# Kernel optimization log

Hardware: AMD Instinct MI355X
Metric: run time of the kernel (lower is better)

## Reference

```python
import jax, jax.numpy as jnp
import numpy as np

N_ENT = 100000
N_USR = 1024
E = 400000
D = 128
H = 4
R = 32


def setup_inputs() -> dict:
    key = jax.random.key(0)
    ks = jax.random.split(key, 9)
    a = float(np.sqrt(6.0 / (D + D)))  # xavier_uniform bound for [D, D]
    return {
        "entity_emb": jax.random.normal(ks[0], (N_ENT, D), dtype=jnp.float32),
        "user_emb": jax.random.normal(ks[1], (N_USR, D), dtype=jnp.float32),
        "interact_mat": jnp.zeros((1,), dtype=jnp.float32),  # unused by forward
        "weight": jax.random.normal(ks[2], (R, D), dtype=jnp.float32) * 0.1,
        "qTrans": jax.random.uniform(ks[3], (D, D), minval=-a, maxval=a, dtype=jnp.float32),
        "kTrans": jax.random.uniform(ks[4], (D, D), minval=-a, maxval=a, dtype=jnp.float32),
        "vTrans": jax.random.uniform(ks[5], (D, D), minval=-a, maxval=a, dtype=jnp.float32),
        "edge_index": jax.random.randint(ks[6], (2, E), 0, N_ENT, dtype=jnp.int64)
            if jax.config.jax_enable_x64 else jax.random.randint(ks[6], (2, E), 0, N_ENT, dtype=jnp.int32),
        "edge_type": jax.random.randint(ks[7], (E,), 1, R + 1, dtype=jnp.int32),  # types in [1, R]
        "layer": 0,
    }


def _kglayer(rows, col_embeds, embeds, n_seg, qT, kT, vT):
    # rows: [E] target-node index, col_embeds: [E, D] edge messages
    dh = D // H
    row_embeds = embeds[rows]                              # gather [E, D]
    q = (row_embeds @ qT).reshape(-1, H, dh)
    k = (col_embeds @ kT).reshape(-1, H, dh)
    v = (col_embeds @ vT).reshape(-1, H, dh)
    att = jnp.clip(jnp.einsum("ehd,ehd->eh", q, k), -10.0, 10.0)
    exp_att = jnp.exp(att)                                 # [E, H]
    att_norm = jax.ops.segment_sum(exp_att, rows, num_segments=n_seg)[rows]
    att = exp_att / (att_norm + 1e-8)
    res = (att[..., None] * v).reshape(-1, D)              # [E, D]
    return jax.ops.segment_sum(res, rows, num_segments=n_seg)


def _sim_hrt(head_emb, tail_emb, rel_emb):
    # per-edge scalar attention logit [E, 1]
    tr = jnp.linalg.norm(tail_emb * rel_emb, axis=1, keepdims=True)
    hr = jnp.linalg.norm(head_emb * rel_emb, axis=1, keepdims=True)
    return (hr * tr) ** 2


def reference(entity_emb, user_emb, interact_mat, weight, qTrans, kTrans, vTrans,
              edge_index, edge_type, layer):
    n_entities = entity_emb.shape[0]
    head, tail = edge_index[0], edge_index[1]
    rel = weight[edge_type - 1]                            # [E, D]
    neigh = entity_emb[tail] * rel                         # [E, D]
    kg_emb = _kglayer(head, neigh, entity_emb, n_entities, qTrans, kTrans, vTrans)
    w = _sim_hrt(kg_emb[head], kg_emb[tail], rel)          # [E, 1]
    w = jnp.broadcast_to(w, neigh.shape)                   # expand to [E, D]
    # scatter_softmax over edges sharing the same head (numerically stable)
    m = jax.ops.segment_max(w, head, num_segments=n_entities)[head]
    e = jnp.exp(w - m)
    s = jax.ops.segment_sum(e, head, num_segments=n_entities)[head]
    soft = e / s
    msg = soft * entity_emb[tail]
    return jax.ops.segment_sum(msg, head, num_segments=n_entities)
```

## Files before the change

### kernel.cpp

```cpp
#include <hip/hip_runtime.h>
#include <cstdint>

#define D 128
#define H 4
#define N_ENT 100000
#define N_EDGE 400000
#define R 32

#define SCAN_NB ((N_ENT + 511) / 512)

__global__ void k_hist(const int* __restrict__ head, int* __restrict__ deg) {
  const int e = blockIdx.x * 256 + threadIdx.x;
  if (e < N_EDGE) atomicAdd(&deg[head[e]], 1);
}

__global__ __launch_bounds__(256) void k_scan1(const int* __restrict__ deg,
                                               int* __restrict__ bsum) {
  const int t = threadIdx.x;
  const int i = blockIdx.x * 512 + t * 2;
  int v0 = (i < N_ENT) ? deg[i] : 0;
  int v1 = (i + 1 < N_ENT) ? deg[i + 1] : 0;
  int s = v0 + v1;
#pragma unroll
  for (int k = 1; k < 64; k <<= 1) s += __shfl_xor(s, k);
  __shared__ int ws[4];
  if ((t & 63) == 0) ws[t >> 6] = s;
  __syncthreads();
  if (t == 0) bsum[blockIdx.x] = ws[0] + ws[1] + ws[2] + ws[3];
}

__global__ __launch_bounds__(256) void k_scan2(const int* __restrict__ bsum,
                                               int* __restrict__ bbase,
                                               int* __restrict__ off) {
  __shared__ int sh[256];
  const int t = threadIdx.x;
  const int v = (t < SCAN_NB) ? bsum[t] : 0;
  sh[t] = v;
  __syncthreads();
  for (int d = 1; d < 256; d <<= 1) {
    const int u = (t >= d) ? sh[t - d] : 0;
    __syncthreads();
    sh[t] += u;
    __syncthreads();
  }
  if (t < SCAN_NB) bbase[t] = sh[t] - v;
  if (t == SCAN_NB - 1) off[N_ENT] = sh[t];
}

__global__ __launch_bounds__(256) void k_scan3(const int* __restrict__ deg,
                                               const int* __restrict__ bbase,
                                               int* __restrict__ off,
                                               int* __restrict__ cur) {
  __shared__ int sh[256];
  const int t = threadIdx.x;
  const int i = blockIdx.x * 512 + t * 2;
  const int v0 = (i < N_ENT) ? deg[i] : 0;
  const int v1 = (i + 1 < N_ENT) ? deg[i + 1] : 0;
  const int s = v0 + v1;
  sh[t] = s;
  __syncthreads();
  for (int d = 1; d < 256; d <<= 1) {
    const int u = (t >= d) ? sh[t - d] : 0;
    __syncthreads();
    sh[t] += u;
    __syncthreads();
  }
  const int ex = sh[t] - s + bbase[blockIdx.x];
  if (i < N_ENT) {
    off[i] = ex;
    cur[i] = ex;
  }
  if (i + 1 < N_ENT) {
    off[i + 1] = ex + v0;
    cur[i + 1] = ex + v0;
  }
}

__global__ void k_scatter(const int* __restrict__ head,
                          const int* __restrict__ tail,
                          const int* __restrict__ etype, int* __restrict__ cur,
                          int2* __restrict__ teP) {
  const int e = blockIdx.x * 256 + threadIdx.x;
  if (e >= N_EDGE) return;
  const int hd = head[e];
  const int pos = atomicAdd(&cur[hd], 1);
  teP[pos] = make_int2(tail[e], etype[e] - 1);
}

__global__ __launch_bounds__(256) void k_tr(const float* __restrict__ in,
                                            float* __restrict__ out) {
  __shared__ float tile[32][33];
  const int bx = blockIdx.x & 3, by = blockIdx.x >> 2;
  const int c = threadIdx.x & 31;
  const int r0 = (threadIdx.x >> 5) * 4;
#pragma unroll
  for (int i = 0; i < 4; ++i)
    tile[r0 + i][c] = in[(by * 32 + r0 + i) * 128 + bx * 32 + c];
  __syncthreads();
#pragma unroll
  for (int i = 0; i < 4; ++i)
    out[(bx * 32 + r0 + i) * 128 + by * 32 + c] = tile[c][r0 + i];
}

__global__ __launch_bounds__(512) void k_qproj(const float* __restrict__ ent,
                                               const float* __restrict__ qT,
                                               float* __restrict__ Q) {
  __shared__ float sT[D * D];
  __shared__ float rows[D * 128];
  const int t = threadIdx.x;
  const int n0 = blockIdx.x * 128;
#pragma unroll
  for (int s = 0; s < 8; ++s) {
    const int idx = (s * 512 + t) * 4;
    *(float4*)&sT[idx] = *(const float4*)&qT[idx];
  }
  {
    const int g = t & 3;
    const int n = t >> 2;
    const int node = n0 + n;
    if (node < N_ENT) {
      const float* src = ent + (size_t)node * D;
#pragma unroll
      for (int s = 0; s < 8; ++s) {
        const int i = s * 16 + g * 4;
        float4 v = *(const float4*)&src[i];
        rows[(i + 0) * 128 + n] = v.x;
        rows[(i + 1) * 128 + n] = v.y;
        rows[(i + 2) * 128 + n] = v.z;
        rows[(i + 3) * 128 + n] = v.w;
      }
    } else {
#pragma unroll
      for (int s = 0; s < 8; ++s) {
        const int i = s * 16 + g * 4;
        rows[(i + 0) * 128 + n] = 0.f;
        rows[(i + 1) * 128 + n] = 0.f;
        rows[(i + 2) * 128 + n] = 0.f;
        rows[(i + 3) * 128 + n] = 0.f;
      }
    }
  }
  __syncthreads();
  const int jj = t & 15;
  const int ee = t >> 4;
  float acc[4][8];
#pragma unroll
  for (int a = 0; a < 4; ++a)
#pragma unroll
    for (int b = 0; b < 8; ++b) acc[a][b] = 0.f;
#pragma unroll 4
  for (int i = 0; i < D; ++i) {
    float4 b0 = *(float4*)&sT[i * D + jj * 8];
    float4 b1 = *(float4*)&sT[i * D + jj * 8 + 4];
    float4 a0 = *(float4*)&rows[i * 128 + ee * 4];
    float bv[8] = {b0.x, b0.y, b0.z, b0.w, b1.x, b1.y, b1.z, b1.w};
    float av[4] = {a0.x, a0.y, a0.z, a0.w};
#pragma unroll
    for (int a = 0; a < 4; ++a)
#pragma unroll
      for (int b = 0; b < 8; ++b) acc[a][b] = fmaf(av[a], bv[b], acc[a][b]);
  }
#pragma unroll
  for (int a = 0; a < 4; ++a) {
    const int node = n0 + ee * 4 + a;
    if (node < N_ENT) {
      float4 o0 = {acc[a][0], acc[a][1], acc[a][2], acc[a][3]};
      float4 o1 = {acc[a][4], acc[a][5], acc[a][6], acc[a][7]};
      *(float4*)&Q[(size_t)node * D + jj * 8] = o0;
      *(float4*)&Q[(size_t)node * D + jj * 8 + 4] = o1;
    }
  }
}

__global__ __launch_bounds__(256, 8) void k_fused(
    const float* __restrict__ ent, const float* __restrict__ wrel,
    const float* __restrict__ kTt, const float* __restrict__ vT, float* qkg,
    const int* __restrict__ off, const int2* __restrict__ teP) {
  __shared__ float sQ[8 * 128];
  __shared__ float sPA[8 * 512];
  const int t = threadIdx.x;
  const int base = blockIdx.x * 8;

  const int wid = t >> 6;
  const int half = (t >> 5) & 1;
  const int l32 = t & 31;
  const int kk = wid * 2 + half;
  const int n = base + kk;

  {
    const int k = t >> 5;
    const int c4 = (t & 31) * 4;
    *(float4*)&sQ[k * 128 + c4] =
        *(const float4*)&qkg[(size_t)(base + k) * D + c4];
  }

  const int eb = off[n];
  const int deg = off[n + 1] - eb;
  float4 xv = {0, 0, 0, 0}, rv = {0, 0, 0, 0};
  if (deg > 0) {
    const int2 pf = teP[eb];
    xv = *(const float4*)&ent[(size_t)pf.x * D + l32 * 4];
    rv = *(const float4*)&wrel[(size_t)pf.y * D + l32 * 4];
  }
  __syncthreads();

  {
    const int i = t & 127;
    const int sub = t >> 7;
    float pp[2][8];
#pragma unroll
    for (int hh = 0; hh < 2; ++hh)
#pragma unroll
      for (int k = 0; k < 8; ++k) pp[hh][k] = 0.f;
#pragma unroll
    for (int hh = 0; hh < 2; ++hh) {
      const int h = sub * 2 + hh;
#pragma unroll 2
      for (int c4 = 0; c4 < 8; ++c4) {
        const float kv0 = kTt[(h * 32 + c4 * 4 + 0) * 128 + i];
        const float kv1 = kTt[(h * 32 + c4 * 4 + 1) * 128 + i];
        const float kv2 = kTt[(h * 32 + c4 * 4 + 2) * 128 + i];
        const float kv3 = kTt[(h * 32 + c4 * 4 + 3) * 128 + i];
#pragma unroll
        for (int k = 0; k < 8; ++k) {
          const float4 q = *(const float4*)&sQ[k * 128 + h * 32 + c4 * 4];
          pp[hh][k] = fmaf(kv0, q.x, pp[hh][k]);
          pp[hh][k] = fmaf(kv1, q.y, pp[hh][k]);
          pp[hh][k] = fmaf(kv2, q.z, pp[hh][k]);
          pp[hh][k] = fmaf(kv3, q.w, pp[hh][k]);
        }
      }
    }
#pragma unroll
    for (int hh = 0; hh < 2; ++hh)
#pragma unroll
      for (int k = 0; k < 8; ++k)
        sPA[k * 512 + (sub * 2 + hh) * 128 + i] = pp[hh][k];
  }
  __syncthreads();

  {
    const int lp = l32 & 3;
    const float4 P0 = *(const float4*)&sPA[kk * 512 + 0 * 128 + l32 * 4];
    const float4 P1 = *(const float4*)&sPA[kk * 512 + 1 * 128 + l32 * 4];
    const float4 P2 = *(const float4*)&sPA[kk * 512 + 2 * 128 + l32 * 4];
    const float4 P3 = *(const float4*)&sPA[kk * 512 + 3 * 128 + l32 * 4];
    float4 b0 = {0, 0, 0, 0}, b1 = {0, 0, 0, 0};
    float4 b2 = {0, 0, 0, 0}, b3 = {0, 0, 0, 0};
    float s0 = 0.f, s1 = 0.f, s2 = 0.f, s3 = 0.f;
    for (int idx = 0; idx < deg; ++idx) {
      const float4 cx = xv, cr = rv;
      if (idx + 1 < deg) {
        const int2 pf = teP[eb + idx + 1];
        xv = *(const float4*)&ent[(size_t)pf.x * D + l32 * 4];
        rv = *(const float4*)&wrel[(size_t)pf.y * D + l32 * 4];
      }
      const float4 nh = {cx.x * cr.x, cx.y * cr.y, cx.z * cr.z, cx.w * cr.w};
      float d0 = nh.x * P0.x + nh.y * P0.y + nh.z * P0.z + nh.w * P0.w;
      float d1 = nh.x * P1.x + nh.y * P1.y + nh.z * P1.z + nh.w * P1.w;
      float d2 = nh.x * P2.x + nh.y * P2.y + nh.z * P2.z + nh.w * P2.w;
      float d3 = nh.x * P3.x + nh.y * P3.y + nh.z * P3.z + nh.w * P3.w;
      float x01 = (l32 & 1) ? d1 : d0;
      float y01 = (l32 & 1) ? d0 : d1;
      x01 += __shfl_xor(y01, 1);
      float x23 = (l32 & 1) ? d3 : d2;
      float y23 = (l32 & 1) ? d2 : d3;
      x23 += __shfl_xor(y23, 1);
      float xa = (l32 & 2) ? x23 : x01;
      float xb = (l32 & 2) ? x01 : x23;
      xa += __shfl_xor(xb, 2);
      xa += __shfl_xor(xa, 4);
      xa += __shfl_xor(xa, 8);
      xa += __shfl_xor(xa, 16);
      const float eL = __expf(fminf(fmaxf(xa, -10.f), 10.f));
      const float e0 = eL;
      const float e1 = __shfl_xor(eL, 1);
      const float e2 = __shfl_xor(eL, 2);
      const float e3 = __shfl_xor(eL, 3);
      b0.x = fmaf(e0, nh.x, b0.x); b0.y = fmaf(e0, nh.y, b0.y);
      b0.z = fmaf(e0, nh.z, b0.z); b0.w = fmaf(e0, nh.w, b0.w);
      b1.x = fmaf(e1, nh.x, b1.x); b1.y = fmaf(e1, nh.y, b1.y);
      b1.z = fmaf(e1, nh.z, b1.z); b1.w = fmaf(e1, nh.w, b1.w);
      b2.x = fmaf(e2, nh.x, b2.x); b2.y = fmaf(e2, nh.y, b2.y);
      b2.z = fmaf(e2, nh.z, b2.z); b2.w = fmaf(e2, nh.w, b2.w);
      b3.x = fmaf(e3, nh.x, b3.x); b3.y = fmaf(e3, nh.y, b3.y);
      b3.z = fmaf(e3, nh.z, b3.z); b3.w = fmaf(e3, nh.w, b3.w);
      s0 += e0; s1 += e1; s2 += e2; s3 += e3;
    }
    const float i0 = 1.f / (s0 + 1e-8f);
    const float i1 = 1.f / (s1 + 1e-8f);
    const float i2 = 1.f / (s2 + 1e-8f);
    const float i3 = 1.f / (s3 + 1e-8f);
    float4 o0 = {b0.x * i0, b0.y * i0, b0.z * i0, b0.w * i0};
    float4 o1 = {b1.x * i1, b1.y * i1, b1.z * i1, b1.w * i1};
    float4 o2 = {b2.x * i2, b2.y * i2, b2.z * i2, b2.w * i2};
    float4 o3 = {b3.x * i3, b3.y * i3, b3.z * i3, b3.w * i3};
    const int sb = kk * 512 + l32 * 4;
    *(float4*)&sPA[sb + ((lp ^ 0) << 7)] = o0;
    *(float4*)&sPA[sb + ((lp ^ 1) << 7)] = o1;
    *(float4*)&sPA[sb + ((lp ^ 2) << 7)] = o2;
    *(float4*)&sPA[sb + ((lp ^ 3) << 7)] = o3;
  }
  __syncthreads();

  {
    const int c = t & 127;
    const int g4 = (t >> 7) * 4;
    const int h = c >> 5;
    float acc0 = 0.f, acc1 = 0.f, acc2 = 0.f, acc3 = 0.f;
    const float* agg0 = &sPA[(g4 + 0) * 512 + h * 128];
    const float* agg1 = &sPA[(g4 + 1) * 512 + h * 128];
    const float* agg2 = &sPA[(g4 + 2) * 512 + h * 128];
    const float* agg3 = &sPA[(g4 + 3) * 512 + h * 128];
#pragma unroll 4
    for (int d4 = 0; d4 < 32; ++d4) {
      const float4 a0 = *(const float4*)&agg0[d4 * 4];
      const float4 a1 = *(const float4*)&agg1[d4 * 4];
      const float4 a2 = *(const float4*)&agg2[d4 * 4];
      const float4 a3 = *(const float4*)&agg3[d4 * 4];
      const float v0 = vT[(d4 * 4 + 0) * 128 + c];
      const float v1 = vT[(d4 * 4 + 1) * 128 + c];
      const float v2 = vT[(d4 * 4 + 2) * 128 + c];
      const float v3 = vT[(d4 * 4 + 3) * 128 + c];
      acc0 = fmaf(a0.x, v0, acc0); acc0 = fmaf(a0.y, v1, acc0);
      acc0 = fmaf(a0.z, v2, acc0); acc0 = fmaf(a0.w, v3, acc0);
      acc1 = fmaf(a1.x, v0, acc1); acc1 = fmaf(a1.y, v1, acc1);
      acc1 = fmaf(a1.z, v2, acc1); acc1 = fmaf(a1.w, v3, acc1);
      acc2 = fmaf(a2.x, v0, acc2); acc2 = fmaf(a2.y, v1, acc2);
      acc2 = fmaf(a2.z, v2, acc2); acc2 = fmaf(a2.w, v3, acc2);
      acc3 = fmaf(a3.x, v0, acc3); acc3 = fmaf(a3.y, v1, acc3);
      acc3 = fmaf(a3.z, v2, acc3); acc3 = fmaf(a3.w, v3, acc3);
    }
    qkg[(size_t)(base + g4 + 0) * D + c] = acc0;
    qkg[(size_t)(base + g4 + 1) * D + c] = acc1;
    qkg[(size_t)(base + g4 + 2) * D + c] = acc2;
    qkg[(size_t)(base + g4 + 3) * D + c] = acc3;
  }
}

__global__ __launch_bounds__(256) void k_S(const float* __restrict__ kg,
                                           const float* __restrict__ wrel,
                                           float* __restrict__ S) {
  __shared__ float sB[D * 32];
  __shared__ float sA[D * 64];
  const int t = threadIdx.x;
  const int n0 = blockIdx.x * 64;
  {
    const int r = t & 31;
    const int qg = t >> 5;
#pragma unroll
    for (int s = 0; s < 4; ++s) {
      const int d = qg * 16 + s * 4;
      float4 b = *(const float4*)&wrel[(size_t)r * D + d];
      sB[(d + 0) * 32 + r] = b.x * b.x;
      sB[(d + 1) * 32 + r] = b.y * b.y;
      sB[(d + 2) * 32 + r] = b.z * b.z;
      sB[(d + 3) * 32 + r] = b.w * b.w;
    }
  }
  {
    const int nn = t & 63;
    const int dg = t >> 6;
    const int node = n0 + nn;
#pragma unroll
    for (int s = 0; s < 8; ++s) {
      const int d = dg * 32 + s * 4;
      float4 a = {0, 0, 0, 0};
      if (node < N_ENT) a = *(const float4*)&kg[(size_t)node * D + d];
      sA[(d + 0) * 64 + nn] = a.x * a.x;
      sA[(d + 1) * 64 + nn] = a.y * a.y;
      sA[(d + 2) * 64 + nn] = a.z * a.z;
      sA[(d + 3) * 64 + nn] = a.w * a.w;
    }
  }
  __syncthreads();
  const int nn2 = t >> 2;
  const int rg = t & 3;
  float acc[8];
#pragma unroll
  for (int c = 0; c < 8; ++c) acc[c] = 0.f;
#pragma unroll 4
  for (int d = 0; d < D; ++d) {
    const float a = sA[d * 64 + nn2];
    float4 b0 = *(float4*)&sB[d * 32 + rg * 8];
    float4 b1 = *(float4*)&sB[d * 32 + rg * 8 + 4];
    acc[0] = fmaf(a, b0.x, acc[0]);
    acc[1] = fmaf(a, b0.y, acc[1]);
    acc[2] = fmaf(a, b0.z, acc[2]);
    acc[3] = fmaf(a, b0.w, acc[3]);
    acc[4] = fmaf(a, b1.x, acc[4]);
    acc[5] = fmaf(a, b1.y, acc[5]);
    acc[6] = fmaf(a, b1.z, acc[6]);
    acc[7] = fmaf(a, b1.w, acc[7]);
  }
  const int node = n0 + nn2;
  if (node < N_ENT) {
    float4 o0 = {acc[0], acc[1], acc[2], acc[3]};
    float4 o1 = {acc[4], acc[5], acc[6], acc[7]};
    *(float4*)&S[(size_t)node * 32 + rg * 8] = o0;
    *(float4*)&S[(size_t)node * 32 + rg * 8 + 4] = o1;
  }
}

__global__ __launch_bounds__(256) void k_out2(
    const float* __restrict__ ent, const float* __restrict__ S,
    const int* __restrict__ off, const int2* __restrict__ teP,
    float* __restrict__ out) {
  const int t = threadIdx.x;
  const int wid = t >> 6;
  const int lane = t & 63;
  const int n = blockIdx.x * 4 + wid;
  if (n >= N_ENT) return;
  const int eb = off[n];
  const int deg = off[n + 1] - eb;
  float accx = 0.f, accy = 0.f;
  float m = 0.f, ssum = 0.f;
  for (int b = 0; b < deg; b += 64) {
    const int idx = b + lane;
    const bool val = idx < deg;
    const int e = eb + (val ? idx : 0);
    const int2 tp = teP[e];
    const int tl = tp.x;
    const int ty = tp.y;
    float w = val ? S[(size_t)n * 32 + ty] * S[(size_t)tl * 32 + ty] : -1.f;
    float cm = w;
#pragma unroll
    for (int k = 1; k < 64; k <<= 1) cm = fmaxf(cm, __shfl_xor(cm, k));
    const float mnew = fmaxf(m, cm);
    const float scale = __expf(m - mnew);
    const float el = val ? __expf(w - mnew) : 0.f;
    float cs = el;
#pragma unroll
    for (int k = 1; k < 64; k <<= 1) cs += __shfl_xor(cs, k);
    ssum = ssum * scale + cs;
    accx *= scale;
    accy *= scale;
    const int cnt = (deg - b < 64) ? deg - b : 64;
    {
      const int tl0 = __shfl(tl, 0);
      float2 xr = *(const float2*)&ent[(size_t)tl0 * D + lane * 2];
      for (int j = 0; j < cnt; ++j) {
        const float sj = __shfl(el, j);
        const float2 cx = xr;
        if (j + 1 < cnt) {
          const int tlj = __shfl(tl, j + 1);
          xr = *(const float2*)&ent[(size_t)tlj * D + lane * 2];
        }
        accx = fmaf(sj, cx.x, accx);
        accy = fmaf(sj, cx.y, accy);
      }
    }
    m = mnew;
  }
  const float inv = (deg > 0) ? 1.f / ssum : 0.f;
  float2 o = {accx * inv, accy * inv};
  *(float2*)&out[(size_t)n * D + lane * 2] = o;
}

extern "C" void kernel_launch(void* const* d_in, const int* in_sizes, int n_in,
                              void* d_out, int out_size, void* d_ws,
                              size_t ws_size, hipStream_t stream) {
  const float* ent = (const float*)d_in[0];
  const float* wrel = (const float*)d_in[3];
  const float* qT = (const float*)d_in[4];
  const float* kT = (const float*)d_in[5];
  const float* vT = (const float*)d_in[6];
  const int* eidx = (const int*)d_in[7];
  const int* etype = (const int*)d_in[8];
  const int* head = eidx;
  const int* tail = eidx + N_EDGE;

  float* S = (float*)d_ws;
  int* off = (int*)(S + (size_t)N_ENT * 32);
  int* cur = off + (N_ENT + 2);
  int* deg = cur + N_ENT;
  int* bsum = deg + N_ENT;
  int* bbase = bsum + SCAN_NB;
  int2* teP = (int2*)(bbase + SCAN_NB);
  float* kTt = (float*)(teP + N_EDGE);
  float* qkg = (float*)d_out;

  hipMemsetAsync(deg, 0, N_ENT * sizeof(int), stream);
  k_hist<<<(N_EDGE + 255) / 256, 256, 0, stream>>>(head, deg);
  k_scan1<<<SCAN_NB, 256, 0, stream>>>(deg, bsum);
  k_scan2<<<1, 256, 0, stream>>>(bsum, bbase, off);
  k_scan3<<<SCAN_NB, 256, 0, stream>>>(deg, bbase, off, cur);
  k_scatter<<<(N_EDGE + 255) / 256, 256, 0, stream>>>(head, tail, etype, cur,
                                                      teP);
  k_tr<<<16, 256, 0, stream>>>(kT, kTt);
  k_qproj<<<(N_ENT + 127) / 128, 512, 0, stream>>>(ent, qT, qkg);
  k_fused<<<N_ENT / 8, 256, 0, stream>>>(ent, wrel, kTt, vT, qkg, off, teP);
  k_S<<<(N_ENT + 63) / 64, 256, 0, stream>>>(qkg, wrel, S);
  k_out2<<<(N_ENT + 3) / 4, 256, 0, stream>>>(ent, S, off, teP, qkg);
}
```

Baseline: 512.1 us.

## Fuse Q projection and relation-score kernel into main fused attention kernel

Removes the separate Q-projection kernel and the S (kg²·rel²) kernel and computes both inside k_fused per block of 8 nodes. Q is computed from entity rows in shared memory using qT read from global, and S is computed right after kg from squared values kept in shared memory. A small prep kernel transposes kT and precomputes squared relation weights. This avoids writing Q and kg to global and reading them back, plus two launches. In exchange k_fused does more per-block work with global qT reads, and its occupancy hint drops from 8 to 4 blocks.

Result: slower. 577.7 us (+12.8%).

```diff
diff --git a/kernel.cpp b/kernel.cpp
--- a/kernel.cpp
+++ b/kernel.cpp
@@ -87,95 +87,40 @@
   teP[pos] = make_int2(tail[e], etype[e] - 1);
 }
 
-__global__ __launch_bounds__(256) void k_tr(const float* __restrict__ in,
-                                            float* __restrict__ out) {
-  __shared__ float tile[32][33];
-  const int bx = blockIdx.x & 3, by = blockIdx.x >> 2;
-  const int c = threadIdx.x & 31;
-  const int r0 = (threadIdx.x >> 5) * 4;
-#pragma unroll
-  for (int i = 0; i < 4; ++i)
-    tile[r0 + i][c] = in[(by * 32 + r0 + i) * 128 + bx * 32 + c];
-  __syncthreads();
-#pragma unroll
-  for (int i = 0; i < 4; ++i)
-    out[(bx * 32 + r0 + i) * 128 + by * 32 + c] = tile[c][r0 + i];
-}
-
-__global__ __launch_bounds__(512) void k_qproj(const float* __restrict__ ent,
-                                               const float* __restrict__ qT,
-                                               float* __restrict__ Q) {
-  __shared__ float sT[D * D];
-  __shared__ float rows[D * 128];
-  const int t = threadIdx.x;
-  const int n0 = blockIdx.x * 128;
-#pragma unroll
-  for (int s = 0; s < 8; ++s) {
-    const int idx = (s * 512 + t) * 4;
-    *(float4*)&sT[idx] = *(const float4*)&qT[idx];
-  }
-  {
-    const int g = t & 3;
-    const int n = t >> 2;
-    const int node = n0 + n;
-    if (node < N_ENT) {
-      const float* src = ent + (size_t)node * D;
-#pragma unroll
-      for (int s = 0; s < 8; ++s) {
-        const int i = s * 16 + g * 4;
-        float4 v = *(const float4*)&src[i];
-        rows[(i + 0) * 128 + n] = v.x;
-        rows[(i + 1) * 128 + n] = v.y;
-        rows[(i + 2) * 128 + n] = v.z;
-        rows[(i + 3) * 128 + n] = v.w;
-      }
-    } else {
-#pragma unroll
-      for (int s = 0; s < 8; ++s) {
-        const int i = s * 16 + g * 4;
-        rows[(i + 0) * 128 + n] = 0.f;
-        rows[(i + 1) * 128 + n] = 0.f;
-        rows[(i + 2) * 128 + n] = 0.f;
-        rows[(i + 3) * 128 + n] = 0.f;
-      }
-    }
-  }
-  __syncthreads();
-  const int jj = t & 15;
-  const int ee = t >> 4;
-  float acc[4][8];
-#pragma unroll
-  for (int a = 0; a < 4; ++a)
-#pragma unroll
-    for (int b = 0; b < 8; ++b) acc[a][b] = 0.f;
-#pragma unroll 4
-  for (int i = 0; i < D; ++i) {
-    float4 b0 = *(float4*)&sT[i * D + jj * 8];
-    float4 b1 = *(float4*)&sT[i * D + jj * 8 + 4];
-    float4 a0 = *(float4*)&rows[i * 128 + ee * 4];
-    float bv[8] = {b0.x, b0.y, b0.z, b0.w, b1.x, b1.y, b1.z, b1.w};
-    float av[4] = {a0.x, a0.y, a0.z, a0.w};
-#pragma unroll
-    for (int a = 0; a < 4; ++a)
-#pragma unroll
-      for (int b = 0; b < 8; ++b) acc[a][b] = fmaf(av[a], bv[b], acc[a][b]);
-  }
-#pragma unroll
-  for (int a = 0; a < 4; ++a) {
-    const int node = n0 + ee * 4 + a;
-    if (node < N_ENT) {
-      float4 o0 = {acc[a][0], acc[a][1], acc[a][2], acc[a][3]};
-      float4 o1 = {acc[a][4], acc[a][5], acc[a][6], acc[a][7]};
-      *(float4*)&Q[(size_t)node * D + jj * 8] = o0;
-      *(float4*)&Q[(size_t)node * D + jj * 8 + 4] = o1;
-    }
-  }
-}
-
-__global__ __launch_bounds__(256, 8) void k_fused(
+__global__ __launch_bounds__(256) void k_prep(const float* __restrict__ kT,
+                                              float* __restrict__ kTt,
+                                              const float* __restrict__ wrel,
+                                              float* __restrict__ wrel2) {
+  if (blockIdx.x < 16) {
+    __shared__ float tile[32][33];
+    const int bx = blockIdx.x & 3, by = blockIdx.x >> 2;
+    const int c = threadIdx.x & 31;
+    const int r0 = (threadIdx.x >> 5) * 4;
+#pragma unroll
+    for (int i = 0; i < 4; ++i)
+      tile[r0 + i][c] = kT[(by * 32 + r0 + i) * 128 + bx * 32 + c];
+    __syncthreads();
+#pragma unroll
+    for (int i = 0; i < 4; ++i)
+      kTt[(bx * 32 + r0 + i) * 128 + by * 32 + c] = tile[c][r0 + i];
+  } else {
+    const int t = threadIdx.x;
+#pragma unroll
+    for (int s = 0; s < 4; ++s) {
+      const int idx = (s * 256 + t) * 4;
+      float4 v = *(const float4*)&wrel[idx];
+      v.x *= v.x; v.y *= v.y; v.z *= v.z; v.w *= v.w;
+      *(float4*)&wrel2[idx] = v;
+    }
+  }
+}
+
+__global__ __launch_bounds__(256, 4) void k_fused(
     const float* __restrict__ ent, const float* __restrict__ wrel,
-    const float* __restrict__ kTt, const float* __restrict__ vT, float* qkg,
-    const int* __restrict__ off, const int2* __restrict__ teP) {
+    const float* __restrict__ qT, const float* __restrict__ kTt,
+    const float* __restrict__ vT, const float* __restrict__ wrel2,
+    float* __restrict__ S, const int* __restrict__ off,
+    const int2* __restrict__ teP) {
   __shared__ float sQ[8 * 128];
   __shared__ float sPA[8 * 512];
   const int t = threadIdx.x;
@@ -190,8 +135,8 @@
   {
     const int k = t >> 5;
     const int c4 = (t & 31) * 4;
-    *(float4*)&sQ[k * 128 + c4] =
-        *(const float4*)&qkg[(size_t)(base + k) * D + c4];
+    *(float4*)&sPA[k * 128 + c4] =
+        *(const float4*)&ent[(size_t)(base + k) * D + c4];
   }
 
   const int eb = off[n];
@@ -201,6 +146,40 @@
     const int2 pf = teP[eb];
     xv = *(const float4*)&ent[(size_t)pf.x * D + l32 * 4];
     rv = *(const float4*)&wrel[(size_t)pf.y * D + l32 * 4];
+  }
+  __syncthreads();
+
+  {
+    const int j = t & 127;
+    const int g4 = (t >> 7) * 4;
+    const float* sE0 = &sPA[(g4 + 0) * 128];
+    const float* sE1 = &sPA[(g4 + 1) * 128];
+    const float* sE2 = &sPA[(g4 + 2) * 128];
+    const float* sE3 = &sPA[(g4 + 3) * 128];
+    float q0 = 0.f, q1 = 0.f, q2 = 0.f, q3 = 0.f;
+#pragma unroll 4
+    for (int c4 = 0; c4 < 32; ++c4) {
+      const float4 e0 = *(const float4*)&sE0[c4 * 4];
+      const float4 e1 = *(const float4*)&sE1[c4 * 4];
+      const float4 e2 = *(const float4*)&sE2[c4 * 4];
+      const float4 e3 = *(const float4*)&sE3[c4 * 4];
+      const float t0 = qT[(c4 * 4 + 0) * 128 + j];
+      const float t1 = qT[(c4 * 4 + 1) * 128 + j];
+      const float t2 = qT[(c4 * 4 + 2) * 128 + j];
+      const float t3 = qT[(c4 * 4 + 3) * 128 + j];
+      q0 = fmaf(e0.x, t0, q0); q0 = fmaf(e0.y, t1, q0);
+      q0 = fmaf(e0.z, t2, q0); q0 = fmaf(e0.w, t3, q0);
+      q1 = fmaf(e1.x, t0, q1); q1 = fmaf(e1.y, t1, q1);
+      q1 = fmaf(e1.z, t2, q1); q1 = fmaf(e1.w, t3, q1);
+      q2 = fmaf(e2.x, t0, q2); q2 = fmaf(e2.y, t1, q2);
+      q2 = fmaf(e2.z, t2, q2); q2 = fmaf(e2.w, t3, q2);
+      q3 = fmaf(e3.x, t0, q3); q3 = fmaf(e3.y, t1, q3);
+      q3 = fmaf(e3.z, t2, q3); q3 = fmaf(e3.w, t3, q3);
+    }
+    sQ[(g4 + 0) * 128 + j] = q0;
+    sQ[(g4 + 1) * 128 + j] = q1;
+    sQ[(g4 + 2) * 128 + j] = q2;
+    sQ[(g4 + 3) * 128 + j] = q3;
   }
   __syncthreads();
 
@@ -231,6 +210,7 @@
         }
       }
     }
+    __syncthreads();
 #pragma unroll
     for (int hh = 0; hh < 2; ++hh)
 #pragma unroll
@@ -249,13 +229,12 @@
     float4 b2 = {0, 0, 0, 0}, b3 = {0, 0, 0, 0};
     float s0 = 0.f, s1 = 0.f, s2 = 0.f, s3 = 0.f;
     for (int idx = 0; idx < deg; ++idx) {
-      const float4 cx = xv, cr = rv;
+      const float4 nh = {xv.x * rv.x, xv.y * rv.y, xv.z * rv.z, xv.w * rv.w};
       if (idx + 1 < deg) {
         const int2 pf = teP[eb + idx + 1];
         xv = *(const float4*)&ent[(size_t)pf.x * D + l32 * 4];
         rv = *(const float4*)&wrel[(size_t)pf.y * D + l32 * 4];
       }
-      const float4 nh = {cx.x * cr.x, cx.y * cr.y, cx.z * cr.z, cx.w * cr.w};
       float d0 = nh.x * P0.x + nh.y * P0.y + nh.z * P0.z + nh.w * P0.w;
       float d1 = nh.x * P1.x + nh.y * P1.y + nh.z * P1.z + nh.w * P1.w;
       float d2 = nh.x * P2.x + nh.y * P2.y + nh.z * P2.z + nh.w * P2.w;
@@ -331,74 +310,27 @@
       acc3 = fmaf(a3.x, v0, acc3); acc3 = fmaf(a3.y, v1, acc3);
       acc3 = fmaf(a3.z, v2, acc3); acc3 = fmaf(a3.w, v3, acc3);
     }
-    qkg[(size_t)(base + g4 + 0) * D + c] = acc0;
-    qkg[(size_t)(base + g4 + 1) * D + c] = acc1;
-    qkg[(size_t)(base + g4 + 2) * D + c] = acc2;
-    qkg[(size_t)(base + g4 + 3) * D + c] = acc3;
-  }
-}
-
-__global__ __launch_bounds__(256) void k_S(const float* __restrict__ kg,
-                                           const float* __restrict__ wrel,
-                                           float* __restrict__ S) {
-  __shared__ float sB[D * 32];
-  __shared__ float sA[D * 64];
-  const int t = threadIdx.x;
-  const int n0 = blockIdx.x * 64;
-  {
+    sQ[(g4 + 0) * 128 + c] = acc0 * acc0;
+    sQ[(g4 + 1) * 128 + c] = acc1 * acc1;
+    sQ[(g4 + 2) * 128 + c] = acc2 * acc2;
+    sQ[(g4 + 3) * 128 + c] = acc3 * acc3;
+  }
+  __syncthreads();
+
+  {
+    const int nn = t >> 5;
     const int r = t & 31;
-    const int qg = t >> 5;
-#pragma unroll
-    for (int s = 0; s < 4; ++s) {
-      const int d = qg * 16 + s * 4;
-      float4 b = *(const float4*)&wrel[(size_t)r * D + d];
-      sB[(d + 0) * 32 + r] = b.x * b.x;
-      sB[(d + 1) * 32 + r] = b.y * b.y;
-      sB[(d + 2) * 32 + r] = b.z * b.z;
-      sB[(d + 3) * 32 + r] = b.w * b.w;
-    }
-  }
-  {
-    const int nn = t & 63;
-    const int dg = t >> 6;
-    const int node = n0 + nn;
-#pragma unroll
-    for (int s = 0; s < 8; ++s) {
-      const int d = dg * 32 + s * 4;
-      float4 a = {0, 0, 0, 0};
-      if (node < N_ENT) a = *(const float4*)&kg[(size_t)node * D + d];
-      sA[(d + 0) * 64 + nn] = a.x * a.x;
-      sA[(d + 1) * 64 + nn] = a.y * a.y;
-      sA[(d + 2) * 64 + nn] = a.z * a.z;
-      sA[(d + 3) * 64 + nn] = a.w * a.w;
-    }
-  }
-  __syncthreads();
-  const int nn2 = t >> 2;
-  const int rg = t & 3;
-  float acc[8];
-#pragma unroll
-  for (int c = 0; c < 8; ++c) acc[c] = 0.f;
+    const float* kg2 = &sQ[nn * 128];
+    const float* w2 = &wrel2[r * 128];
+    float acc = 0.f;
 #pragma unroll 4
-  for (int d = 0; d < D; ++d) {
-    const float a = sA[d * 64 + nn2];
-    float4 b0 = *(float4*)&sB[d * 32 + rg * 8];
-    float4 b1 = *(float4*)&sB[d * 32 + rg * 8 + 4];
-    acc[0] = fmaf(a, b0.x, acc[0]);
-    acc[1] = fmaf(a, b0.y, acc[1]);
-    acc[2] = fmaf(a, b0.z, acc[2]);
-    acc[3] = fmaf(a, b0.w, acc[3]);
-    acc[4] = fmaf(a, b1.x, acc[4]);
-    acc[5] = fmaf(a, b1.y, acc[5]);
-    acc[6] = fmaf(a, b1.z, acc[6]);
-    acc[7] = fmaf(a, b1.w, acc[7]);
-  }
-  const int node = n0 + nn2;
-  if (node < N_ENT) {
-    float4 o0 = {acc[0], acc[1], acc[2], acc[3]};
-    float4 o1 = {acc[4], acc[5], acc[6], acc[7]};
-    *(float4*)&S[(size_t)node * 32 + rg * 8] = o0;
-    *(float4*)&S[(size_t)node * 32 + rg * 8 + 4] = o1;
+    for (int c4 = 0; c4 < 32; ++c4) {
+      const float4 a = *(const float4*)&kg2[c4 * 4];
+      const float4 b = *(const float4*)&w2[c4 * 4];
+      acc = fmaf(a.x, b.x, acc); acc = fmaf(a.y, b.y, acc);
+      acc = fmaf(a.z, b.z, acc); acc = fmaf(a.w, b.w, acc);
+    }
+    S[(size_t)(base + nn) * 32 + r] = acc;
   }
 }
 
@@ -478,7 +410,8 @@
   int* bbase = bsum + SCAN_NB;
   int2* teP = (int2*)(bbase + SCAN_NB);
   float* kTt = (float*)(teP + N_EDGE);
-  float* qkg = (float*)d_out;
+  float* wrel2 = (float*)cur;
+  float* out = (float*)d_out;
 
   hipMemsetAsync(deg, 0, N_ENT * sizeof(int), stream);
   k_hist<<<(N_EDGE + 255) / 256, 256, 0, stream>>>(head, deg);
@@ -487,9 +420,8 @@
   k_scan3<<<SCAN_NB, 256, 0, stream>>>(deg, bbase, off, cur);
   k_scatter<<<(N_EDGE + 255) / 256, 256, 0, stream>>>(head, tail, etype, cur,
                                                       teP);
-  k_tr<<<16, 256, 0, stream>>>(kT, kTt);
-  k_qproj<<<(N_ENT + 127) / 128, 512, 0, stream>>>(ent, qT, qkg);
-  k_fused<<<N_ENT / 8, 256, 0, stream>>>(ent, wrel, kTt, vT, qkg, off, teP);
-  k_S<<<(N_ENT + 63) / 64, 256, 0, stream>>>(qkg, wrel, S);
-  k_out2<<<(N_ENT + 3) / 4, 256, 0, stream>>>(ent, S, off, teP, qkg);
-}
+  k_prep<<<17, 256, 0, stream>>>(kT, kTt, wrel, wrel2);
+  k_fused<<<N_ENT / 8, 256, 0, stream>>>(ent, wrel, qT, kTt, vT, wrel2, S,
+                                         off, teP);
+  k_out2<<<(N_ENT + 3) / 4, 256, 0, stream>>>(ent, S, off, teP, out);
+}
```

## Fuse S computation into k_fused with one wave per node

Applied to the files above, without the earlier changes.

Merges the separate k_S kernel into k_fused. The squared kg rows stay in shared memory and are dotted with a precomputed squared relation table (wrel2, built in a merged prep kernel), so the kg round trip through global memory is avoided. k_fused now uses 512 threads with one 64-lane wave per node and float2 gathers, instead of half-waves with float4. This raises parallelism per node but shortens each gather, and the S dot product is less register-blocked than before. wrel2 reuses the cur buffer, which is dead after the scatter.

Result: slower. 627.2 us (+22.5%).

```diff
diff --git a/kernel.cpp b/kernel.cpp
--- a/kernel.cpp
+++ b/kernel.cpp
@@ -87,19 +87,32 @@
   teP[pos] = make_int2(tail[e], etype[e] - 1);
 }
 
-__global__ __launch_bounds__(256) void k_tr(const float* __restrict__ in,
-                                            float* __restrict__ out) {
-  __shared__ float tile[32][33];
-  const int bx = blockIdx.x & 3, by = blockIdx.x >> 2;
-  const int c = threadIdx.x & 31;
-  const int r0 = (threadIdx.x >> 5) * 4;
-#pragma unroll
-  for (int i = 0; i < 4; ++i)
-    tile[r0 + i][c] = in[(by * 32 + r0 + i) * 128 + bx * 32 + c];
-  __syncthreads();
-#pragma unroll
-  for (int i = 0; i < 4; ++i)
-    out[(bx * 32 + r0 + i) * 128 + by * 32 + c] = tile[c][r0 + i];
+__global__ __launch_bounds__(256) void k_prep(const float* __restrict__ kT,
+                                              float* __restrict__ kTt,
+                                              const float* __restrict__ wrel,
+                                              float* __restrict__ wrel2) {
+  if (blockIdx.x < 16) {
+    __shared__ float tile[32][33];
+    const int bx = blockIdx.x & 3, by = blockIdx.x >> 2;
+    const int c = threadIdx.x & 31;
+    const int r0 = (threadIdx.x >> 5) * 4;
+#pragma unroll
+    for (int i = 0; i < 4; ++i)
+      tile[r0 + i][c] = kT[(by * 32 + r0 + i) * 128 + bx * 32 + c];
+    __syncthreads();
+#pragma unroll
+    for (int i = 0; i < 4; ++i)
+      kTt[(bx * 32 + r0 + i) * 128 + by * 32 + c] = tile[c][r0 + i];
+  } else {
+    const int t = threadIdx.x;
+#pragma unroll
+    for (int s = 0; s < 4; ++s) {
+      const int idx = (s * 256 + t) * 4;
+      float4 v = *(const float4*)&wrel[idx];
+      v.x *= v.x; v.y *= v.y; v.z *= v.z; v.w *= v.w;
+      *(float4*)&wrel2[idx] = v;
+    }
+  }
 }
 
 __global__ __launch_bounds__(512) void k_qproj(const float* __restrict__ ent,
@@ -172,233 +185,157 @@
   }
 }
 
-__global__ __launch_bounds__(256, 8) void k_fused(
+__global__ __launch_bounds__(512, 8) void k_fused(
     const float* __restrict__ ent, const float* __restrict__ wrel,
-    const float* __restrict__ kTt, const float* __restrict__ vT, float* qkg,
-    const int* __restrict__ off, const int2* __restrict__ teP) {
+    const float* __restrict__ kTt, const float* __restrict__ vT,
+    const float* __restrict__ wrel2, const float* __restrict__ qkg,
+    float* __restrict__ S, const int* __restrict__ off,
+    const int2* __restrict__ teP) {
   __shared__ float sQ[8 * 128];
   __shared__ float sPA[8 * 512];
   const int t = threadIdx.x;
   const int base = blockIdx.x * 8;
-
-  const int wid = t >> 6;
-  const int half = (t >> 5) & 1;
-  const int l32 = t & 31;
-  const int kk = wid * 2 + half;
+  const int kk = t >> 6;
+  const int lane = t & 63;
   const int n = base + kk;
 
-  {
-    const int k = t >> 5;
-    const int c4 = (t & 31) * 4;
-    *(float4*)&sQ[k * 128 + c4] =
-        *(const float4*)&qkg[(size_t)(base + k) * D + c4];
-  }
+  *(float2*)&sQ[kk * 128 + lane * 2] =
+      *(const float2*)&qkg[(size_t)n * D + lane * 2];
 
   const int eb = off[n];
   const int deg = off[n + 1] - eb;
-  float4 xv = {0, 0, 0, 0}, rv = {0, 0, 0, 0};
+  float2 xv = {0, 0}, rv = {0, 0};
   if (deg > 0) {
     const int2 pf = teP[eb];
-    xv = *(const float4*)&ent[(size_t)pf.x * D + l32 * 4];
-    rv = *(const float4*)&wrel[(size_t)pf.y * D + l32 * 4];
+    xv = *(const float2*)&ent[(size_t)pf.x * D + lane * 2];
+    rv = *(const float2*)&wrel[(size_t)pf.y * D + lane * 2];
   }
   __syncthreads();
 
   {
     const int i = t & 127;
-    const int sub = t >> 7;
-    float pp[2][8];
-#pragma unroll
-    for (int hh = 0; hh < 2; ++hh)
-#pragma unroll
-      for (int k = 0; k < 8; ++k) pp[hh][k] = 0.f;
-#pragma unroll
-    for (int hh = 0; hh < 2; ++hh) {
-      const int h = sub * 2 + hh;
+    const int h = t >> 7;
+    float pp[8];
+#pragma unroll
+    for (int k = 0; k < 8; ++k) pp[k] = 0.f;
 #pragma unroll 2
-      for (int c4 = 0; c4 < 8; ++c4) {
-        const float kv0 = kTt[(h * 32 + c4 * 4 + 0) * 128 + i];
-        const float kv1 = kTt[(h * 32 + c4 * 4 + 1) * 128 + i];
-        const float kv2 = kTt[(h * 32 + c4 * 4 + 2) * 128 + i];
-        const float kv3 = kTt[(h * 32 + c4 * 4 + 3) * 128 + i];
-#pragma unroll
-        for (int k = 0; k < 8; ++k) {
-          const float4 q = *(const float4*)&sQ[k * 128 + h * 32 + c4 * 4];
-          pp[hh][k] = fmaf(kv0, q.x, pp[hh][k]);
-          pp[hh][k] = fmaf(kv1, q.y, pp[hh][k]);
-          pp[hh][k] = fmaf(kv2, q.z, pp[hh][k]);
-          pp[hh][k] = fmaf(kv3, q.w, pp[hh][k]);
-        }
+    for (int c4 = 0; c4 < 8; ++c4) {
+      const float kv0 = kTt[(h * 32 + c4 * 4 + 0) * 128 + i];
+      const float kv1 = kTt[(h * 32 + c4 * 4 + 1) * 128 + i];
+      const float kv2 = kTt[(h * 32 + c4 * 4 + 2) * 128 + i];
+      const float kv3 = kTt[(h * 32 + c4 * 4 + 3) * 128 + i];
+#pragma unroll
+      for (int k = 0; k < 8; ++k) {
+        const float4 q = *(const float4*)&sQ[k * 128 + h * 32 + c4 * 4];
+        pp[k] = fmaf(kv0, q.x, pp[k]);
+        pp[k] = fmaf(kv1, q.y, pp[k]);
+        pp[k] = fmaf(kv2, q.z, pp[k]);
+        pp[k] = fmaf(kv3, q.w, pp[k]);
       }
     }
 #pragma unroll
-    for (int hh = 0; hh < 2; ++hh)
-#pragma unroll
-      for (int k = 0; k < 8; ++k)
-        sPA[k * 512 + (sub * 2 + hh) * 128 + i] = pp[hh][k];
+    for (int k = 0; k < 8; ++k) sPA[k * 512 + h * 128 + i] = pp[k];
   }
   __syncthreads();
 
   {
-    const int lp = l32 & 3;
-    const float4 P0 = *(const float4*)&sPA[kk * 512 + 0 * 128 + l32 * 4];
-    const float4 P1 = *(const float4*)&sPA[kk * 512 + 1 * 128 + l32 * 4];
-    const float4 P2 = *(const float4*)&sPA[kk * 512 + 2 * 128 + l32 * 4];
-    const float4 P3 = *(const float4*)&sPA[kk * 512 + 3 * 128 + l32 * 4];
-    float4 b0 = {0, 0, 0, 0}, b1 = {0, 0, 0, 0};
-    float4 b2 = {0, 0, 0, 0}, b3 = {0, 0, 0, 0};
+    const int lp = lane & 3;
+    const float2 Pv0 = *(const float2*)&sPA[kk * 512 + 0 * 128 + lane * 2];
+    const float2 Pv1 = *(const float2*)&sPA[kk * 512 + 1 * 128 + lane * 2];
+    const float2 Pv2 = *(const float2*)&sPA[kk * 512 + 2 * 128 + lane * 2];
+    const float2 Pv3 = *(const float2*)&sPA[kk * 512 + 3 * 128 + lane * 2];
+    float2 b0 = {0, 0}, b1 = {0, 0}, b2 = {0, 0}, b3 = {0, 0};
     float s0 = 0.f, s1 = 0.f, s2 = 0.f, s3 = 0.f;
     for (int idx = 0; idx < deg; ++idx) {
-      const float4 cx = xv, cr = rv;
+      const float2 nh = {xv.x * rv.x, xv.y * rv.y};
       if (idx + 1 < deg) {
         const int2 pf = teP[eb + idx + 1];
-        xv = *(const float4*)&ent[(size_t)pf.x * D + l32 * 4];
-        rv = *(const float4*)&wrel[(size_t)pf.y * D + l32 * 4];
+        xv = *(const float2*)&ent[(size_t)pf.x * D + lane * 2];
+        rv = *(const float2*)&wrel[(size_t)pf.y * D + lane * 2];
       }
-      const float4 nh = {cx.x * cr.x, cx.y * cr.y, cx.z * cr.z, cx.w * cr.w};
-      float d0 = nh.x * P0.x + nh.y * P0.y + nh.z * P0.z + nh.w * P0.w;
-      float d1 = nh.x * P1.x + nh.y * P1.y + nh.z * P1.z + nh.w * P1.w;
-      float d2 = nh.x * P2.x + nh.y * P2.y + nh.z * P2.z + nh.w * P2.w;
-      float d3 = nh.x * P3.x + nh.y * P3.y + nh.z * P3.z + nh.w * P3.w;
-      float x01 = (l32 & 1) ? d1 : d0;
-      float y01 = (l32 & 1) ? d0 : d1;
+      float d0 = nh.x * Pv0.x + nh.y * Pv0.y;
+      float d1 = nh.x * Pv1.x + nh.y * Pv1.y;
+      float d2 = nh.x * Pv2.x + nh.y * Pv2.y;
+      float d3 = nh.x * Pv3.x + nh.y * Pv3.y;
+      float x01 = (lane & 1) ? d1 : d0;
+      float y01 = (lane & 1) ? d0 : d1;
       x01 += __shfl_xor(y01, 1);
-      float x23 = (l32 & 1) ? d3 : d2;
-      float y23 = (l32 & 1) ? d2 : d3;
+      float x23 = (lane & 1) ? d3 : d2;
+      float y23 = (lane & 1) ? d2 : d3;
       x23 += __shfl_xor(y23, 1);
-      float xa = (l32 & 2) ? x23 : x01;
-      float xb = (l32 & 2) ? x01 : x23;
+      float xa = (lane & 2) ? x23 : x01;
+      float xb = (lane & 2) ? x01 : x23;
       xa += __shfl_xor(xb, 2);
       xa += __shfl_xor(xa, 4);
       xa += __shfl_xor(xa, 8);
       xa += __shfl_xor(xa, 16);
+      xa += __shfl_xor(xa, 32);
       const float eL = __expf(fminf(fmaxf(xa, -10.f), 10.f));
       const float e0 = eL;
       const float e1 = __shfl_xor(eL, 1);
       const float e2 = __shfl_xor(eL, 2);
       const float e3 = __shfl_xor(eL, 3);
       b0.x = fmaf(e0, nh.x, b0.x); b0.y = fmaf(e0, nh.y, b0.y);
-      b0.z = fmaf(e0, nh.z, b0.z); b0.w = fmaf(e0, nh.w, b0.w);
       b1.x = fmaf(e1, nh.x, b1.x); b1.y = fmaf(e1, nh.y, b1.y);
-      b1.z = fmaf(e1, nh.z, b1.z); b1.w = fmaf(e1, nh.w, b1.w);
       b2.x = fmaf(e2, nh.x, b2.x); b2.y = fmaf(e2, nh.y, b2.y);
-      b2.z = fmaf(e2, nh.z, b2.z); b2.w = fmaf(e2, nh.w, b2.w);
       b3.x = fmaf(e3, nh.x, b3.x); b3.y = fmaf(e3, nh.y, b3.y);
-      b3.z = fmaf(e3, nh.z, b3.z); b3.w = fmaf(e3, nh.w, b3.w);
       s0 += e0; s1 += e1; s2 += e2; s3 += e3;
     }
     const float i0 = 1.f / (s0 + 1e-8f);
     const float i1 = 1.f / (s1 + 1e-8f);
     const float i2 = 1.f / (s2 + 1e-8f);
     const float i3 = 1.f / (s3 + 1e-8f);
-    float4 o0 = {b0.x * i0, b0.y * i0, b0.z * i0, b0.w * i0};
-    float4 o1 = {b1.x * i1, b1.y * i1, b1.z * i1, b1.w * i1};
-    float4 o2 = {b2.x * i2, b2.y * i2, b2.z * i2, b2.w * i2};
-    float4 o3 = {b3.x * i3, b3.y * i3, b3.z * i3, b3.w * i3};
-    const int sb = kk * 512 + l32 * 4;
-    *(float4*)&sPA[sb + ((lp ^ 0) << 7)] = o0;
-    *(float4*)&sPA[sb + ((lp ^ 1) << 7)] = o1;
-    *(float4*)&sPA[sb + ((lp ^ 2) << 7)] = o2;
-    *(float4*)&sPA[sb + ((lp ^ 3) << 7)] = o3;
+    float2 o0 = {b0.x * i0, b0.y * i0};
+    float2 o1 = {b1.x * i1, b1.y * i1};
+    float2 o2 = {b2.x * i2, b2.y * i2};
+    float2 o3 = {b3.x * i3, b3.y * i3};
+    const int sb = kk * 512 + lane * 2;
+    *(float2*)&sPA[sb + ((lp ^ 0) << 7)] = o0;
+    *(float2*)&sPA[sb + ((lp ^ 1) << 7)] = o1;
+    *(float2*)&sPA[sb + ((lp ^ 2) << 7)] = o2;
+    *(float2*)&sPA[sb + ((lp ^ 3) << 7)] = o3;
   }
   __syncthreads();
 
   {
     const int c = t & 127;
-    const int g4 = (t >> 7) * 4;
+    const int p = t >> 7;
     const int h = c >> 5;
-    float acc0 = 0.f, acc1 = 0.f, acc2 = 0.f, acc3 = 0.f;
-    const float* agg0 = &sPA[(g4 + 0) * 512 + h * 128];
-    const float* agg1 = &sPA[(g4 + 1) * 512 + h * 128];
-    const float* agg2 = &sPA[(g4 + 2) * 512 + h * 128];
-    const float* agg3 = &sPA[(g4 + 3) * 512 + h * 128];
+    const float* aggA = &sPA[(p + 0) * 512 + h * 128];
+    const float* aggB = &sPA[(p + 4) * 512 + h * 128];
+    float accA = 0.f, accB = 0.f;
 #pragma unroll 4
     for (int d4 = 0; d4 < 32; ++d4) {
-      const float4 a0 = *(const float4*)&agg0[d4 * 4];
-      const float4 a1 = *(const float4*)&agg1[d4 * 4];
-      const float4 a2 = *(const float4*)&agg2[d4 * 4];
-      const float4 a3 = *(const float4*)&agg3[d4 * 4];
+      const float4 aA = *(const float4*)&aggA[d4 * 4];
+      const float4 aB = *(const float4*)&aggB[d4 * 4];
       const float v0 = vT[(d4 * 4 + 0) * 128 + c];
       const float v1 = vT[(d4 * 4 + 1) * 128 + c];
       const float v2 = vT[(d4 * 4 + 2) * 128 + c];
       const float v3 = vT[(d4 * 4 + 3) * 128 + c];
-      acc0 = fmaf(a0.x, v0, acc0); acc0 = fmaf(a0.y, v1, acc0);
-      acc0 = fmaf(a0.z, v2, acc0); acc0 = fmaf(a0.w, v3, acc0);
-      acc1 = fmaf(a1.x, v0, acc1); acc1 = fmaf(a1.y, v1, acc1);
-      acc1 = fmaf(a1.z, v2, acc1); acc1 = fmaf(a1.w, v3, acc1);
-      acc2 = fmaf(a2.x, v0, acc2); acc2 = fmaf(a2.y, v1, acc2);
-      acc2 = fmaf(a2.z, v2, acc2); acc2 = fmaf(a2.w, v3, acc2);
-      acc3 = fmaf(a3.x, v0, acc3); acc3 = fmaf(a3.y, v1, acc3);
-      acc3 = fmaf(a3.z, v2, acc3); acc3 = fmaf(a3.w, v3, acc3);
-    }
-    qkg[(size_t)(base + g4 + 0) * D + c] = acc0;
-    qkg[(size_t)(base + g4 + 1) * D + c] = acc1;
-    qkg[(size_t)(base + g4 + 2) * D + c] = acc2;
-    qkg[(size_t)(base + g4 + 3) * D + c] = acc3;
-  }
-}
-
-__global__ __launch_bounds__(256) void k_S(const float* __restrict__ kg,
-                                           const float* __restrict__ wrel,
-                                           float* __restrict__ S) {
-  __shared__ float sB[D * 32];
-  __shared__ float sA[D * 64];
-  const int t = threadIdx.x;
-  const int n0 = blockIdx.x * 64;
-  {
+      accA = fmaf(aA.x, v0, accA); accA = fmaf(aA.y, v1, accA);
+      accA = fmaf(aA.z, v2, accA); accA = fmaf(aA.w, v3, accA);
+      accB = fmaf(aB.x, v0, accB); accB = fmaf(aB.y, v1, accB);
+      accB = fmaf(aB.z, v2, accB); accB = fmaf(aB.w, v3, accB);
+    }
+    sQ[(p + 0) * 128 + c] = accA * accA;
+    sQ[(p + 4) * 128 + c] = accB * accB;
+  }
+  __syncthreads();
+
+  if (t < 256) {
+    const int nn = t >> 5;
     const int r = t & 31;
-    const int qg = t >> 5;
-#pragma unroll
-    for (int s = 0; s < 4; ++s) {
-      const int d = qg * 16 + s * 4;
-      float4 b = *(const float4*)&wrel[(size_t)r * D + d];
-      sB[(d + 0) * 32 + r] = b.x * b.x;
-      sB[(d + 1) * 32 + r] = b.y * b.y;
-      sB[(d + 2) * 32 + r] = b.z * b.z;
-      sB[(d + 3) * 32 + r] = b.w * b.w;
-    }
-  }
-  {
-    const int nn = t & 63;
-    const int dg = t >> 6;
-    const int node = n0 + nn;
-#pragma unroll
-    for (int s = 0; s < 8; ++s) {
-      const int d = dg * 32 + s * 4;
-      float4 a = {0, 0, 0, 0};
-      if (node < N_ENT) a = *(const float4*)&kg[(size_t)node * D + d];
-      sA[(d + 0) * 64 + nn] = a.x * a.x;
-      sA[(d + 1) * 64 + nn] = a.y * a.y;
-      sA[(d + 2) * 64 + nn] = a.z * a.z;
-      sA[(d + 3) * 64 + nn] = a.w * a.w;
-    }
-  }
-  __syncthreads();
-  const int nn2 = t >> 2;
-  const int rg = t & 3;
-  float acc[8];
-#pragma unroll
-  for (int c = 0; c < 8; ++c) acc[c] = 0.f;
+    const float* kg2 = &sQ[nn * 128];
+    const float* w2 = &wrel2[r * 128];
+    float acc = 0.f;
 #pragma unroll 4
-  for (int d = 0; d < D; ++d) {
-    const float a = sA[d * 64 + nn2];
-    float4 b0 = *(float4*)&sB[d * 32 + rg * 8];
-    float4 b1 = *(float4*)&sB[d * 32 + rg * 8 + 4];
-    acc[0] = fmaf(a, b0.x, acc[0]);
-    acc[1] = fmaf(a, b0.y, acc[1]);
-    acc[2] = fmaf(a, b0.z, acc[2]);
-    acc[3] = fmaf(a, b0.w, acc[3]);
-    acc[4] = fmaf(a, b1.x, acc[4]);
-    acc[5] = fmaf(a, b1.y, acc[5]);
-    acc[6] = fmaf(a, b1.z, acc[6]);
-    acc[7] = fmaf(a, b1.w, acc[7]);
-  }
-  const int node = n0 + nn2;
-  if (node < N_ENT) {
-    float4 o0 = {acc[0], acc[1], acc[2], acc[3]};
-    float4 o1 = {acc[4], acc[5], acc[6], acc[7]};
-    *(float4*)&S[(size_t)node * 32 + rg * 8] = o0;
-    *(float4*)&S[(size_t)node * 32 + rg * 8 + 4] = o1;
+    for (int c4 = 0; c4 < 32; ++c4) {
+      const float4 a = *(const float4*)&kg2[c4 * 4];
+      const float4 b = *(const float4*)&w2[c4 * 4];
+      acc = fmaf(a.x, b.x, acc); acc = fmaf(a.y, b.y, acc);
+      acc = fmaf(a.z, b.z, acc); acc = fmaf(a.w, b.w, acc);
+    }
+    S[(size_t)(base + nn) * 32 + r] = acc;
   }
 }
 
@@ -478,6 +415,7 @@
   int* bbase = bsum + SCAN_NB;
   int2* teP = (int2*)(bbase + SCAN_NB);
   float* kTt = (float*)(teP + N_EDGE);
+  float* wrel2 = (float*)cur;
   float* qkg = (float*)d_out;
 
   hipMemsetAsync(deg, 0, N_ENT * sizeof(int), stream);
@@ -487,9 +425,9 @@
   k_scan3<<<SCAN_NB, 256, 0, stream>>>(deg, bbase, off, cur);
   k_scatter<<<(N_EDGE + 255) / 256, 256, 0, stream>>>(head, tail, etype, cur,
                                                       teP);
-  k_tr<<<16, 256, 0, stream>>>(kT, kTt);
+  k_prep<<<17, 256, 0, stream>>>(kT, kTt, wrel, wrel2);
   k_qproj<<<(N_ENT + 127) / 128, 512, 0, stream>>>(ent, qT, qkg);
-  k_fused<<<N_ENT / 8, 256, 0, stream>>>(ent, wrel, kTt, vT, qkg, off, teP);
-  k_S<<<(N_ENT + 63) / 64, 256, 0, stream>>>(qkg, wrel, S);
+  k_fused<<<N_ENT / 8, 512, 0, stream>>>(ent, wrel, kTt, vT, wrel2, qkg, S,
+                                         off, teP);
   k_out2<<<(N_ENT + 3) / 4, 256, 0, stream>>>(ent, S, off, teP, qkg);
 }
```
